# Kernel tuning notes

Measured on AMD Instinct MI355X. Metric: run time of the kernel, lower is better.

The kernel has to match this reference:

```python
import jax, jax.numpy as jnp
import numpy as np

N_NODES = 50000
N_EDGES = 500000
D_IN = 128
HID = 128
OUT = 2
N_REL = 4
BN_EPS = 1e-5


def setup_inputs() -> dict:
    key = jax.random.key(0)
    ks = jax.random.split(key, 14)
    s_in = 1.0 / np.sqrt(D_IN)
    s_h = 1.0 / np.sqrt(HID)
    return {
        "x": jax.random.normal(ks[0], (N_NODES, D_IN), jnp.float32),
        "edge_index": jax.random.randint(ks[1], (N_REL, 2, N_EDGES), 0, N_NODES, jnp.int32),
        "W1": jax.random.normal(ks[2], (N_REL, D_IN, HID), jnp.float32) * s_in,
        "b1": jax.random.normal(ks[3], (N_REL, HID), jnp.float32) * s_in,
        "W2": jax.random.normal(ks[4], (N_REL, HID, HID), jnp.float32) * s_h,
        "b2": jax.random.normal(ks[5], (N_REL, HID), jnp.float32) * s_h,
        "bn_gamma": jnp.ones((HID,), jnp.float32),
        "bn_beta": jnp.zeros((HID,), jnp.float32),
        "lin1_W": jax.random.normal(ks[6], (HID, HID), jnp.float32) * s_h,
        "lin1_b": jax.random.normal(ks[7], (HID,), jnp.float32) * s_h,
        "lin2_W": jax.random.normal(ks[8], (HID, OUT), jnp.float32) * s_h,
        "lin2_b": jax.random.normal(ks[9], (OUT,), jnp.float32) * s_h,
    }


def _gcn(x, ei, W, b):
    # GCNConv: D^-1/2 (A + I) D^-1/2 (X W) + b
    n = x.shape[0]
    h = x @ W                                    # [N, H]
    loops = jnp.arange(n, dtype=ei.dtype)
    src = jnp.concatenate([ei[0], loops])        # add self loops
    dst = jnp.concatenate([ei[1], loops])
    deg = jax.ops.segment_sum(jnp.ones(dst.shape, h.dtype), dst, num_segments=n)
    dinv = jnp.where(deg > 0, jax.lax.rsqrt(deg), 0.0)
    norm = dinv[src] * dinv[dst]                 # [E+N]
    msg = h[src] * norm[:, None]                 # gather + scale
    return jax.ops.segment_sum(msg, dst, num_segments=n) + b


def _hetero(x, edge_index, W, b):
    # HeteroConv with aggr='sum' over the 4 relation types (same src/dst node type)
    out = _gcn(x, edge_index[0], W[0], b[0])
    for r in range(1, N_REL):
        out = out + _gcn(x, edge_index[r], W[r], b[r])
    return out


def reference(x, edge_index, W1, b1, W2, b2, bn_gamma, bn_beta, lin1_W, lin1_b, lin2_W, lin2_b):
    h = jax.nn.relu(_hetero(x, edge_index, W1, b1))
    h = jax.nn.relu(_hetero(h, edge_index, W2, b2))
    # BatchNorm1d (batch statistics, biased variance)
    mean = h.mean(axis=0)
    var = h.var(axis=0)
    h = (h - mean) * jax.lax.rsqrt(var + BN_EPS) * bn_gamma + bn_beta
    h = jax.nn.relu(h @ lin1_W + lin1_b)
    # dropout is identity in eval
    return h @ lin2_W + lin2_b
```

## Files before the change

### kernel.cpp

```cpp
#include <hip/hip_runtime.h>
#include <math.h>

#define NN 50000
#define NE 500000
#define NREL 4
#define D 128
#define RSZ 512
#define NRANGE 98
#define NBK (NREL * NRANGE)
#define BCAP 6144
#define NCH 128
#define CH 3907
#define FCAP 96
#define CAST_BLKS 6250
#define TN 32
#define NPW 8
#define NTILE ((NN + TN - 1) / TN)
static constexpr float BN_EPS = 1e-5f;

typedef __attribute__((ext_vector_type(8))) _Float16 half8;
typedef __attribute__((ext_vector_type(4))) float f32x4;

__device__ __forceinline__ unsigned short f2h_bits(float f) {
    _Float16 h = (_Float16)f;
    return __builtin_bit_cast(unsigned short, h);
}
__device__ __forceinline__ float hi2f(unsigned p) {
    return (float)__builtin_bit_cast(_Float16, (unsigned short)(p >> 16));
}

__global__ __launch_bounds__(256) void k_pre(const float* __restrict__ x,
                                             const float* __restrict__ W1, const float* __restrict__ W2,
                                             const float* __restrict__ l1W, const float* __restrict__ b1,
                                             const float* __restrict__ b2,
                                             unsigned short* __restrict__ xb,
                                             unsigned short* __restrict__ Wt1,
                                             unsigned short* __restrict__ Wt2,
                                             unsigned short* __restrict__ Wt3,
                                             float* __restrict__ bs1, float* __restrict__ bs2,
                                             float* __restrict__ bnsum) {
    int blk = blockIdx.x, tid = threadIdx.x;
    if (blk < CAST_BLKS) {
        int i = blk * 256 + tid;
        float4 v = *(const float4*)(x + (size_t)i * 4);
        unsigned short u[4] = {f2h_bits(v.x), f2h_bits(v.y), f2h_bits(v.z), f2h_bits(v.w)};
        *(ushort4*)(xb + (size_t)i * 4) = *(ushort4*)u;
    } else if (blk < CAST_BLKS + 256) {
        int i = (blk - CAST_BLKS) * 256 + tid;
        int kk = i & 511, n = i >> 9;
        Wt1[n * 512 + kk] = f2h_bits(W1[kk * 128 + n]);
        Wt2[n * 512 + kk] = f2h_bits(W2[kk * 128 + n]);
    } else if (blk < CAST_BLKS + 320) {
        int i = (blk - CAST_BLKS - 256) * 256 + tid;
        int kk = i & 127, n = i >> 7;
        Wt3[n * 128 + kk] = f2h_bits(l1W[kk * 128 + n]);
    } else {
        if (tid < 128) {
            bs1[tid] = b1[tid] + b1[128 + tid] + b1[256 + tid] + b1[384 + tid];
            bs2[tid] = b2[tid] + b2[128 + tid] + b2[256 + tid] + b2[384 + tid];
        }
        bnsum[tid] = 0.f;
    }
}

__global__ __launch_bounds__(256) void k_bin(const int* __restrict__ ei,
                                             int* __restrict__ frag,
                                             int* __restrict__ cntg) {
    int c = blockIdx.x, r = blockIdx.y;
    const int* srcp = ei + r * 2 * NE;
    const int* dstp = srcp + NE;
    __shared__ int bins[NRANGE * FCAP];
    __shared__ int cnt[NRANGE];
    int tid = threadIdx.x;
    for (int i = tid; i < NRANGE; i += 256) cnt[i] = 0;
    __syncthreads();
    int e0 = c * CH, e1 = min(e0 + CH, NE);
    for (int e = e0 + tid; e < e1; e += 256) {
        int d = dstp[e];
        int s = srcp[e];
        int q = d >> 9;
        int pos = atomicAdd(&cnt[q], 1);
        if (pos < FCAP) bins[q * FCAP + pos] = s | ((d & 511) << 16);
    }
    __syncthreads();
    int w = tid >> 6, lane = tid & 63;
    for (int q = w; q < NRANGE; q += 4) {
        int k = min(cnt[q], FCAP);
        int gbase = ((r * NRANGE + q) * NCH + c) * FCAP;
        for (int i = lane; i < k; i += 64) frag[gbase + i] = bins[q * FCAP + i];
    }
    for (int q = tid; q < NRANGE; q += 256) cntg[(r * NRANGE + q) * NCH + c] = min(cnt[q], FCAP);
}

__global__ __launch_bounds__(512) void k_sortb(const int* __restrict__ frag,
                                               const int* __restrict__ cntg,
                                               unsigned short* __restrict__ csr,
                                               int* __restrict__ rstart,
                                               int* __restrict__ rend,
                                               float* __restrict__ dinv) {
    int q = blockIdx.x, r = blockIdx.y;
    int blk = r * NRANGE + q;
    int n0 = q * RSZ;
    int nrows = min(RSZ, NN - n0);
    __shared__ int cnts[NCH], cbase[NCH];
    __shared__ int stage[BCAP];
    __shared__ unsigned short csr_s[BCAP];
    __shared__ int hist[RSZ], off[RSZ], cnt2[RSZ];
    int tid = threadIdx.x;
    hist[tid] = 0;
    cnt2[tid] = 0;
    if (tid < NCH) cnts[tid] = cntg[blk * NCH + tid];
    __syncthreads();
    if (tid < NCH) cbase[tid] = cnts[tid];
    __syncthreads();
    for (int d = 1; d < NCH; d <<= 1) {
        int t = 0;
        if (tid < NCH && tid >= d) t = cbase[tid - d];
        __syncthreads();
        if (tid < NCH) cbase[tid] += t;
        __syncthreads();
    }
    if (tid < NCH) cbase[tid] -= cnts[tid];
    __syncthreads();
    int tot = cbase[NCH - 1] + cnts[NCH - 1];
    {
        int g = tid >> 2, l = tid & 3;
        int k = cnts[g], cb = cbase[g];
        int gbase = (blk * NCH + g) * FCAP;
        for (int i = l; i < k; i += 4)
            if (cb + i < BCAP) stage[cb + i] = frag[gbase + i];
    }
    __syncthreads();
    if (tot > BCAP) tot = BCAP;
    for (int i = tid; i < tot; i += 512) atomicAdd(&hist[(stage[i] >> 16) & 511], 1);
    __syncthreads();
    int h = hist[tid];
    if (tid < nrows) dinv[r * NN + n0 + tid] = rsqrtf((float)(h + 1));
    off[tid] = h;
    __syncthreads();
    for (int d = 1; d < RSZ; d <<= 1) {
        int t = (tid >= d) ? off[tid - d] : 0;
        __syncthreads();
        off[tid] += t;
        __syncthreads();
    }
    int excl = off[tid] - h;
    __syncthreads();
    off[tid] = excl;
    int base = blk * BCAP;
    if (tid < nrows) {
        rstart[r * NN + n0 + tid] = base + excl;
        rend[r * NN + n0 + tid] = base + excl + h;
    }
    __syncthreads();
    for (int i = tid; i < tot; i += 512) {
        int v = stage[i];
        int dl = (v >> 16) & 511;
        int p = atomicAdd(&cnt2[dl], 1);
        csr_s[off[dl] + p] = (unsigned short)(v & 0xFFFF);
    }
    __syncthreads();
    for (int i = tid; i < tot; i += 512) csr[base + i] = csr_s[i];
}

__global__ __launch_bounds__(256) void k_wei(const unsigned short* __restrict__ csr,
                                             const float* __restrict__ dinv,
                                             unsigned* __restrict__ wpack) {
    int gi = blockIdx.x * 256 + threadIdx.x;
    int r = gi / (NRANGE * BCAP);
    int s = csr[gi];
    float w = dinv[r * NN + min(s, NN - 1)];
    wpack[gi] = (unsigned)s | ((unsigned)f2h_bits(w) << 16);
}

template <bool STATS>
__global__ __launch_bounds__(256) void k_fused(const unsigned short* __restrict__ in,
                                               const unsigned* __restrict__ wpack,
                                               const int* __restrict__ rstart,
                                               const int* __restrict__ rend,
                                               const float* __restrict__ dinv,
                                               const unsigned short* __restrict__ Bt,
                                               const float* __restrict__ bias,
                                               unsigned short* __restrict__ C,
                                               float* __restrict__ bnsum) {
    __shared__ unsigned short A_s[TN * 512];
    int tid = threadIdx.x;
    int wave = tid >> 6, lane = tid & 63;
    int t = lane & 15;
    int base = lane & 48;
    int q = base >> 4;
    int tile = blockIdx.x;
    const half8* in8 = (const half8*)in;
    int nbq = q * NN;

    int row0 = wave * NPW;
    {
        int n0 = tile * TN + row0;
        int nc0 = min(n0, NN - 1);
        int sP = rstart[nbq + nc0];
        int eP = rend[nbq + nc0];
        float wP = dinv[nbq + nc0];
        half8 uP = in8[(size_t)nc0 * 16 + t];
        for (int i = 0; i < NPW; ++i) {
            int row = row0 + i;
            int n = tile * TN + row;
            bool valid = (n < NN);
            int start = sP;
            int deg = valid ? (eP - sP) : 0;
            float wn = valid ? wP : 0.f;
            half8 us = uP;
            if (i + 1 < NPW) {
                int nn = min(n + 1, NN - 1);
                sP = rstart[nbq + nn];
                eP = rend[nbq + nn];
                wP = dinv[nbq + nn];
                uP = in8[(size_t)nn * 16 + t];
            }
            int dm = deg;
            dm = max(dm, __shfl_xor(dm, 16));
            dm = max(dm, __shfl_xor(dm, 32));
            float a[8];
#pragma unroll
            for (int j = 0; j < 8; j++) a[j] = wn * (float)us[j];

            for (int w0 = 0; w0 < dm; w0 += 16) {
                int li = w0 + t;
                int gi = min(start + li, NBK * BCAP - 1);
                unsigned pv = wpack[gi];
                if (li >= deg) pv = 0u;
                unsigned p0 = __shfl(pv, base + 0), p1 = __shfl(pv, base + 1);
                unsigned p2 = __shfl(pv, base + 2), p3 = __shfl(pv, base + 3);
                unsigned p4 = __shfl(pv, base + 4), p5 = __shfl(pv, base + 5);
                unsigned p6 = __shfl(pv, base + 6), p7 = __shfl(pv, base + 7);
                {
                    half8 r0 = in8[(p0 & 0xFFFFu) * 16 + t];
                    half8 r1 = in8[(p1 & 0xFFFFu) * 16 + t];
                    half8 r2 = in8[(p2 & 0xFFFFu) * 16 + t];
                    half8 r3 = in8[(p3 & 0xFFFFu) * 16 + t];
                    half8 r4 = in8[(p4 & 0xFFFFu) * 16 + t];
                    half8 r5 = in8[(p5 & 0xFFFFu) * 16 + t];
                    half8 r6 = in8[(p6 & 0xFFFFu) * 16 + t];
                    half8 r7 = in8[(p7 & 0xFFFFu) * 16 + t];
                    float w0f = hi2f(p0), w1f = hi2f(p1), w2f = hi2f(p2), w3f = hi2f(p3);
                    float w4f = hi2f(p4), w5f = hi2f(p5), w6f = hi2f(p6), w7f = hi2f(p7);
#pragma unroll
                    for (int j = 0; j < 8; j++) a[j] = fmaf((float)r0[j], w0f, a[j]);
#pragma unroll
                    for (int j = 0; j < 8; j++) a[j] = fmaf((float)r1[j], w1f, a[j]);
#pragma unroll
                    for (int j = 0; j < 8; j++) a[j] = fmaf((float)r2[j], w2f, a[j]);
#pragma unroll
                    for (int j = 0; j < 8; j++) a[j] = fmaf((float)r3[j], w3f, a[j]);
#pragma unroll
                    for (int j = 0; j < 8; j++) a[j] = fmaf((float)r4[j], w4f, a[j]);
#pragma unroll
                    for (int j = 0; j < 8; j++) a[j] = fmaf((float)r5[j], w5f, a[j]);
#pragma unroll
                    for (int j = 0; j < 8; j++) a[j] = fmaf((float)r6[j], w6f, a[j]);
#pragma unroll
                    for (int j = 0; j < 8; j++) a[j] = fmaf((float)r7[j], w7f, a[j]);
                }
                if (w0 + 8 >= dm) continue;
                p0 = __shfl(pv, base + 8);  p1 = __shfl(pv, base + 9);
                p2 = __shfl(pv, base + 10); p3 = __shfl(pv, base + 11);
                p4 = __shfl(pv, base + 12); p5 = __shfl(pv, base + 13);
                p6 = __shfl(pv, base + 14); p7 = __shfl(pv, base + 15);
                {
                    half8 r0 = in8[(p0 & 0xFFFFu) * 16 + t];
                    half8 r1 = in8[(p1 & 0xFFFFu) * 16 + t];
                    half8 r2 = in8[(p2 & 0xFFFFu) * 16 + t];
                    half8 r3 = in8[(p3 & 0xFFFFu) * 16 + t];
                    half8 r4 = in8[(p4 & 0xFFFFu) * 16 + t];
                    half8 r5 = in8[(p5 & 0xFFFFu) * 16 + t];
                    half8 r6 = in8[(p6 & 0xFFFFu) * 16 + t];
                    half8 r7 = in8[(p7 & 0xFFFFu) * 16 + t];
                    float w0f = hi2f(p0), w1f = hi2f(p1), w2f = hi2f(p2), w3f = hi2f(p3);
                    float w4f = hi2f(p4), w5f = hi2f(p5), w6f = hi2f(p6), w7f = hi2f(p7);
#pragma unroll
                    for (int j = 0; j < 8; j++) a[j] = fmaf((float)r0[j], w0f, a[j]);
#pragma unroll
                    for (int j = 0; j < 8; j++) a[j] = fmaf((float)r1[j], w1f, a[j]);
#pragma unroll
                    for (int j = 0; j < 8; j++) a[j] = fmaf((float)r2[j], w2f, a[j]);
#pragma unroll
                    for (int j = 0; j < 8; j++) a[j] = fmaf((float)r3[j], w3f, a[j]);
#pragma unroll
                    for (int j = 0; j < 8; j++) a[j] = fmaf((float)r4[j], w4f, a[j]);
#pragma unroll
                    for (int j = 0; j < 8; j++) a[j] = fmaf((float)r5[j], w5f, a[j]);
#pragma unroll
                    for (int j = 0; j < 8; j++) a[j] = fmaf((float)r6[j], w6f, a[j]);
#pragma unroll
                    for (int j = 0; j < 8; j++) a[j] = fmaf((float)r7[j], w7f, a[j]);
                }
            }
            _Float16 ob[8];
#pragma unroll
            for (int j = 0; j < 8; j++) ob[j] = (_Float16)(wn * a[j]);
            int offb = row * 1024 + ((lane * 16) ^ ((row & 7) << 4));
            *(half8*)((char*)A_s + offb) = *(half8*)ob;
        }
    }
    __syncthreads();

    int ln = lane & 15, quad = lane >> 4;
    f32x4 acc[2][2];
#pragma unroll
    for (int a = 0; a < 2; a++)
#pragma unroll
        for (int b = 0; b < 2; b++) acc[a][b] = (f32x4){0.f, 0.f, 0.f, 0.f};
    size_t brow[2];
#pragma unroll
    for (int nf = 0; nf < 2; nf++) brow[nf] = (size_t)(wave * 32 + nf * 16 + ln) * 512;

    for (int k0 = 0; k0 < 512; k0 += 32) {
        int kofb = k0 * 2 + quad * 16;
        half8 af[2], bf[2];
#pragma unroll
        for (int mf = 0; mf < 2; mf++) {
            int rr = mf * 16 + ln;
            int offb = rr * 1024 + (kofb ^ ((rr & 7) << 4));
            af[mf] = *(const half8*)((const char*)A_s + offb);
        }
#pragma unroll
        for (int nf = 0; nf < 2; nf++) bf[nf] = *(const half8*)(Bt + brow[nf] + (kofb >> 1));
#pragma unroll
        for (int mf = 0; mf < 2; mf++)
#pragma unroll
            for (int nf = 0; nf < 2; nf++)
                acc[mf][nf] = __builtin_amdgcn_mfma_f32_16x16x32_f16(af[mf], bf[nf], acc[mf][nf], 0, 0, 0);
    }

    float bs[2];
#pragma unroll
    for (int nf = 0; nf < 2; nf++) bs[nf] = bias[wave * 32 + nf * 16 + ln];
    float sn[2] = {0.f, 0.f}, qn[2] = {0.f, 0.f};
#pragma unroll
    for (int mf = 0; mf < 2; mf++)
#pragma unroll
        for (int nf = 0; nf < 2; nf++)
#pragma unroll
            for (int rg = 0; rg < 4; rg++) {
                int m = tile * TN + mf * 16 + quad * 4 + rg;
                if (m < NN) {
                    float v = fmaxf(acc[mf][nf][rg] + bs[nf], 0.f);
                    if (STATS) { sn[nf] += v; qn[nf] += v * v; }
                    C[(size_t)m * 128 + wave * 32 + nf * 16 + ln] = f2h_bits(v);
                }
            }
    if (STATS) {
#pragma unroll
        for (int nf = 0; nf < 2; nf++) {
            float s = sn[nf], qq = qn[nf];
            s += __shfl_xor(s, 16); s += __shfl_xor(s, 32);
            qq += __shfl_xor(qq, 16); qq += __shfl_xor(qq, 32);
            if (quad == 0) {
                int col = wave * 32 + nf * 16 + ln;
                unsafeAtomicAdd(&bnsum[col], s);
                unsafeAtomicAdd(&bnsum[128 + col], qq);
            }
        }
    }
}

__global__ __launch_bounds__(256) void k_final(const unsigned short* __restrict__ R2,
                                               const float* __restrict__ bnsum,
                                               const float* __restrict__ gamma,
                                               const float* __restrict__ beta,
                                               const unsigned short* __restrict__ Wt3,
                                               const float* __restrict__ l1b,
                                               const float* __restrict__ l2W,
                                               const float* __restrict__ l2b,
                                               float* __restrict__ out) {
    __shared__ float bnp_s[256];
    int tid = threadIdx.x;
    if (tid < 128) {
        float mean = bnsum[tid] / (float)NN;
        float var = bnsum[128 + tid] / (float)NN - mean * mean;
        float sc = gamma[tid] * rsqrtf(var + BN_EPS);
        bnp_s[tid] = sc;
        bnp_s[128 + tid] = beta[tid] - mean * sc;
    }
    __syncthreads();
    int w = tid >> 6, lane = tid & 63;
    int ln = lane & 15, quad = lane >> 4;
    int mwave = blockIdx.x * 256 + w * 64;

    f32x4 acc[4][8];
#pragma unroll
    for (int a = 0; a < 4; a++)
#pragma unroll
        for (int b = 0; b < 8; b++) acc[a][b] = (f32x4){0.f, 0.f, 0.f, 0.f};

    size_t arow[4];
#pragma unroll
    for (int mf = 0; mf < 4; mf++) {
        int m = mwave + mf * 16 + ln;
        arow[mf] = (size_t)min(m, NN - 1) * 128;
    }
    size_t brow[8];
#pragma unroll
    for (int nf = 0; nf < 8; nf++) brow[nf] = (size_t)(nf * 16 + ln) * 128;

    for (int k0 = 0; k0 < 128; k0 += 32) {
        int kof = k0 + quad * 8;
        float scv[8], shv[8];
#pragma unroll
        for (int j = 0; j < 8; j++) {
            scv[j] = bnp_s[kof + j];
            shv[j] = bnp_s[128 + kof + j];
        }
        half8 af[4], bf[8];
#pragma unroll
        for (int mf = 0; mf < 4; mf++) {
            half8 rv = *(const half8*)(R2 + arow[mf] + kof);
            _Float16 ab[8];
#pragma unroll
            for (int j = 0; j < 8; j++)
                ab[j] = (_Float16)(fmaf((float)rv[j], scv[j], shv[j]));
            af[mf] = *(half8*)ab;
        }
#pragma unroll
        for (int nf = 0; nf < 8; nf++) bf[nf] = *(const half8*)(Wt3 + brow[nf] + kof);
#pragma unroll
        for (int mf = 0; mf < 4; mf++)
#pragma unroll
            for (int nf = 0; nf < 8; nf++)
                acc[mf][nf] = __builtin_amdgcn_mfma_f32_16x16x32_f16(af[mf], bf[nf], acc[mf][nf], 0, 0, 0);
    }

    float b1v[8], w0[8], w1[8];
#pragma unroll
    for (int nf = 0; nf < 8; nf++) {
        int n = nf * 16 + ln;
        b1v[nf] = l1b[n];
        w0[nf] = l2W[n * 2];
        w1[nf] = l2W[n * 2 + 1];
    }
    float ob0 = l2b[0], ob1 = l2b[1];
#pragma unroll
    for (int mf = 0; mf < 4; mf++)
#pragma unroll
        for (int rg = 0; rg < 4; rg++) {
            float p0 = 0.f, p1 = 0.f;
#pragma unroll
            for (int nf = 0; nf < 8; nf++) {
                float y = fmaxf(acc[mf][nf][rg] + b1v[nf], 0.f);
                p0 += y * w0[nf];
                p1 += y * w1[nf];
            }
            p0 += __shfl_xor(p0, 1); p0 += __shfl_xor(p0, 2);
            p0 += __shfl_xor(p0, 4); p0 += __shfl_xor(p0, 8);
            p1 += __shfl_xor(p1, 1); p1 += __shfl_xor(p1, 2);
            p1 += __shfl_xor(p1, 4); p1 += __shfl_xor(p1, 8);
            int m = mwave + mf * 16 + quad * 4 + rg;
            if (ln == 0 && m < NN) {
                out[(size_t)m * 2 + 0] = p0 + ob0;
                out[(size_t)m * 2 + 1] = p1 + ob1;
            }
        }
}

extern "C" void kernel_launch(void* const* d_in, const int* in_sizes, int n_in,
                              void* d_out, int out_size, void* d_ws, size_t ws_size,
                              hipStream_t stream) {
    const float* x = (const float*)d_in[0];
    const int* ei = (const int*)d_in[1];
    const float* W1 = (const float*)d_in[2];
    const float* b1 = (const float*)d_in[3];
    const float* W2 = (const float*)d_in[4];
    const float* b2 = (const float*)d_in[5];
    const float* gamma = (const float*)d_in[6];
    const float* beta = (const float*)d_in[7];
    const float* l1W = (const float*)d_in[8];
    const float* l1b = (const float*)d_in[9];
    const float* l2W = (const float*)d_in[10];
    const float* l2b = (const float*)d_in[11];
    float* out = (float*)d_out;

    char* ws = (char*)d_ws;
    size_t off = 0;
    auto alloc = [&](size_t bytes) {
        void* p = ws + off;
        off += (bytes + 255) & ~(size_t)255;
        return p;
    };
    float* dinv = (float*)alloc((size_t)NREL * NN * sizeof(float));
    int* rstart = (int*)alloc((size_t)NREL * NN * sizeof(int));
    int* rend = (int*)alloc((size_t)NREL * NN * sizeof(int));
    unsigned short* csr = (unsigned short*)alloc((size_t)NBK * BCAP * 2);
    unsigned* wpack = (unsigned*)alloc((size_t)NBK * BCAP * 4);
    unsigned short* xb = (unsigned short*)alloc((size_t)NN * D * 2);
    unsigned short* h1b = (unsigned short*)alloc((size_t)NN * D * 2);
    unsigned short* R2b = (unsigned short*)alloc((size_t)NN * D * 2);
    unsigned short* Wt1 = (unsigned short*)alloc(128 * 512 * 2);
    unsigned short* Wt2 = (unsigned short*)alloc(128 * 512 * 2);
    unsigned short* Wt3 = (unsigned short*)alloc(128 * 128 * 2);
    float* bs1 = (float*)alloc(128 * sizeof(float));
    float* bs2 = (float*)alloc(128 * sizeof(float));
    float* bnsum = (float*)alloc(256 * sizeof(float));
    int* frag = (int*)alloc((size_t)NREL * NRANGE * NCH * FCAP * 4);
    int* cntg = (int*)alloc((size_t)NREL * NRANGE * NCH * 4);

    k_pre<<<CAST_BLKS + 321, 256, 0, stream>>>(x, W1, W2, l1W, b1, b2, xb, Wt1, Wt2, Wt3,
                                               bs1, bs2, bnsum);
    dim3 bgrid(NCH, NREL);
    k_bin<<<bgrid, 256, 0, stream>>>(ei, frag, cntg);
    dim3 sgrid(NRANGE, NREL);
    k_sortb<<<sgrid, 512, 0, stream>>>(frag, cntg, csr, rstart, rend, dinv);
    k_wei<<<(NBK * BCAP) / 256, 256, 0, stream>>>(csr, dinv, wpack);

    k_fused<false><<<NTILE, 256, 0, stream>>>(xb, wpack, rstart, rend, dinv, Wt1, bs1, h1b, nullptr);
    k_fused<true><<<NTILE, 256, 0, stream>>>(h1b, wpack, rstart, rend, dinv, Wt2, bs2, R2b, bnsum);
    k_final<<<(NN + 255) / 256, 256, 0, stream>>>(R2b, bnsum, gamma, beta, Wt3, l1b, l2W, l2b, out);
}
```

Before: 358.9 us.

## Halve fused aggregate-GEMM node tile and prefetch first edge chunk of next node

Shrinks the fused gather+GEMM tile from 32 to 16 nodes per block (4 nodes per wave), doubling the block count. Removes bounds checks because 50000 divides evenly by 16. Prefetches the first wpack edge word for the next node along with its row metadata, to hide load latency in the gather loop. The smaller tile raises parallelism and load balance, but each block does half the MFMA work while still reloading the full B matrix, so weight traffic per node doubles.

```diff
diff --git a/kernel.cpp b/kernel.cpp
--- a/kernel.cpp
+++ b/kernel.cpp
@@ -13,9 +13,9 @@
 #define CH 3907
 #define FCAP 96
 #define CAST_BLKS 6250
-#define TN 32
-#define NPW 8
-#define NTILE ((NN + TN - 1) / TN)
+#define TN 16
+#define NPW 4
+#define NTILE (NN / TN)
 static constexpr float BN_EPS = 1e-5f;
 
 typedef __attribute__((ext_vector_type(8))) _Float16 half8;
@@ -27,6 +27,22 @@
 }
 __device__ __forceinline__ float hi2f(unsigned p) {
     return (float)__builtin_bit_cast(_Float16, (unsigned short)(p >> 16));
+}
+
+__device__ __forceinline__ void acc8(const half8* __restrict__ in8, int t, int src_lane,
+                                     unsigned pv, float a[8]) {
+    unsigned p[8];
+#pragma unroll
+    for (int e = 0; e < 8; e++) p[e] = __shfl(pv, src_lane + e);
+    half8 r[8];
+#pragma unroll
+    for (int e = 0; e < 8; e++) r[e] = in8[(p[e] & 0xFFFFu) * 16 + t];
+#pragma unroll
+    for (int e = 0; e < 8; e++) {
+        float w = hi2f(p[e]);
+#pragma unroll
+        for (int j = 0; j < 8; j++) a[j] = fmaf((float)r[e][j], w, a[j]);
+    }
 }
 
 __global__ __launch_bounds__(256) void k_pre(const float* __restrict__ x,
@@ -192,143 +208,73 @@
     int tile = blockIdx.x;
     const half8* in8 = (const half8*)in;
     int nbq = q * NN;
-
     int row0 = wave * NPW;
-    {
-        int n0 = tile * TN + row0;
-        int nc0 = min(n0, NN - 1);
-        int sP = rstart[nbq + nc0];
-        int eP = rend[nbq + nc0];
-        float wP = dinv[nbq + nc0];
-        half8 uP = in8[(size_t)nc0 * 16 + t];
-        for (int i = 0; i < NPW; ++i) {
-            int row = row0 + i;
-            int n = tile * TN + row;
-            bool valid = (n < NN);
-            int start = sP;
-            int deg = valid ? (eP - sP) : 0;
-            float wn = valid ? wP : 0.f;
-            half8 us = uP;
-            if (i + 1 < NPW) {
-                int nn = min(n + 1, NN - 1);
-                sP = rstart[nbq + nn];
-                eP = rend[nbq + nn];
-                wP = dinv[nbq + nn];
-                uP = in8[(size_t)nn * 16 + t];
+    int n0 = tile * TN + row0;
+
+    int sP = rstart[nbq + n0];
+    int eP = rend[nbq + n0];
+    float wP = dinv[nbq + n0];
+    half8 uP = in8[(size_t)n0 * 16 + t];
+    unsigned pvP = wpack[min(sP + t, NBK * BCAP - 1)];
+
+    for (int i = 0; i < NPW; ++i) {
+        int row = row0 + i;
+        int n = n0 + i;
+        int start = sP, deg = eP - sP;
+        float wn = wP;
+        half8 us = uP;
+        unsigned pv0 = (t < deg) ? pvP : 0u;
+        if (i + 1 < NPW) {
+            int nn = n + 1;
+            sP = rstart[nbq + nn];
+            eP = rend[nbq + nn];
+            wP = dinv[nbq + nn];
+            uP = in8[(size_t)nn * 16 + t];
+            pvP = wpack[min(sP + t, NBK * BCAP - 1)];
+        }
+        int dm = deg;
+        dm = max(dm, __shfl_xor(dm, 16));
+        dm = max(dm, __shfl_xor(dm, 32));
+        float a[8];
+#pragma unroll
+        for (int j = 0; j < 8; j++) a[j] = wn * (float)us[j];
+
+        for (int w0 = 0; w0 < dm; w0 += 16) {
+            unsigned pv;
+            if (w0 == 0) {
+                pv = pv0;
+            } else {
+                int li = w0 + t;
+                pv = wpack[min(start + li, NBK * BCAP - 1)];
+                if (li >= deg) pv = 0u;
             }
-            int dm = deg;
-            dm = max(dm, __shfl_xor(dm, 16));
-            dm = max(dm, __shfl_xor(dm, 32));
-            float a[8];
-#pragma unroll
-            for (int j = 0; j < 8; j++) a[j] = wn * (float)us[j];
-
-            for (int w0 = 0; w0 < dm; w0 += 16) {
-                int li = w0 + t;
-                int gi = min(start + li, NBK * BCAP - 1);
-                unsigned pv = wpack[gi];
-                if (li >= deg) pv = 0u;
-                unsigned p0 = __shfl(pv, base + 0), p1 = __shfl(pv, base + 1);
-                unsigned p2 = __shfl(pv, base + 2), p3 = __shfl(pv, base + 3);
-                unsigned p4 = __shfl(pv, base + 4), p5 = __shfl(pv, base + 5);
-                unsigned p6 = __shfl(pv, base + 6), p7 = __shfl(pv, base + 7);
-                {
-                    half8 r0 = in8[(p0 & 0xFFFFu) * 16 + t];
-                    half8 r1 = in8[(p1 & 0xFFFFu) * 16 + t];
-                    half8 r2 = in8[(p2 & 0xFFFFu) * 16 + t];
-                    half8 r3 = in8[(p3 & 0xFFFFu) * 16 + t];
-                    half8 r4 = in8[(p4 & 0xFFFFu) * 16 + t];
-                    half8 r5 = in8[(p5 & 0xFFFFu) * 16 + t];
-                    half8 r6 = in8[(p6 & 0xFFFFu) * 16 + t];
-                    half8 r7 = in8[(p7 & 0xFFFFu) * 16 + t];
-                    float w0f = hi2f(p0), w1f = hi2f(p1), w2f = hi2f(p2), w3f = hi2f(p3);
-                    float w4f = hi2f(p4), w5f = hi2f(p5), w6f = hi2f(p6), w7f = hi2f(p7);
-#pragma unroll
-                    for (int j = 0; j < 8; j++) a[j] = fmaf((float)r0[j], w0f, a[j]);
-#pragma unroll
-                    for (int j = 0; j < 8; j++) a[j] = fmaf((float)r1[j], w1f, a[j]);
-#pragma unroll
-                    for (int j = 0; j < 8; j++) a[j] = fmaf((float)r2[j], w2f, a[j]);
-#pragma unroll
-                    for (int j = 0; j < 8; j++) a[j] = fmaf((float)r3[j], w3f, a[j]);
-#pragma unroll
-                    for (int j = 0; j < 8; j++) a[j] = fmaf((float)r4[j], w4f, a[j]);
-#pragma unroll
-                    for (int j = 0; j < 8; j++) a[j] = fmaf((float)r5[j], w5f, a[j]);
-#pragma unroll
-                    for (int j = 0; j < 8; j++) a[j] = fmaf((float)r6[j], w6f, a[j]);
-#pragma unroll
-                    for (int j = 0; j < 8; j++) a[j] = fmaf((float)r7[j], w7f, a[j]);
-                }
-                if (w0 + 8 >= dm) continue;
-                p0 = __shfl(pv, base + 8);  p1 = __shfl(pv, base + 9);
-                p2 = __shfl(pv, base + 10); p3 = __shfl(pv, base + 11);
-                p4 = __shfl(pv, base + 12); p5 = __shfl(pv, base + 13);
-                p6 = __shfl(pv, base + 14); p7 = __shfl(pv, base + 15);
-                {
-                    half8 r0 = in8[(p0 & 0xFFFFu) * 16 + t];
-                    half8 r1 = in8[(p1 & 0xFFFFu) * 16 + t];
-                    half8 r2 = in8[(p2 & 0xFFFFu) * 16 + t];
-                    half8 r3 = in8[(p3 & 0xFFFFu) * 16 + t];
-                    half8 r4 = in8[(p4 & 0xFFFFu) * 16 + t];
-                    half8 r5 = in8[(p5 & 0xFFFFu) * 16 + t];
-                    half8 r6 = in8[(p6 & 0xFFFFu) * 16 + t];
-                    half8 r7 = in8[(p7 & 0xFFFFu) * 16 + t];
-                    float w0f = hi2f(p0), w1f = hi2f(p1), w2f = hi2f(p2), w3f = hi2f(p3);
-                    float w4f = hi2f(p4), w5f = hi2f(p5), w6f = hi2f(p6), w7f = hi2f(p7);
-#pragma unroll
-                    for (int j = 0; j < 8; j++) a[j] = fmaf((float)r0[j], w0f, a[j]);
-#pragma unroll
-                    for (int j = 0; j < 8; j++) a[j] = fmaf((float)r1[j], w1f, a[j]);
-#pragma unroll
-                    for (int j = 0; j < 8; j++) a[j] = fmaf((float)r2[j], w2f, a[j]);
-#pragma unroll
-                    for (int j = 0; j < 8; j++) a[j] = fmaf((float)r3[j], w3f, a[j]);
-#pragma unroll
-                    for (int j = 0; j < 8; j++) a[j] = fmaf((float)r4[j], w4f, a[j]);
-#pragma unroll
-                    for (int j = 0; j < 8; j++) a[j] = fmaf((float)r5[j], w5f, a[j]);
-#pragma unroll
-                    for (int j = 0; j < 8; j++) a[j] = fmaf((float)r6[j], w6f, a[j]);
-#pragma unroll
-                    for (int j = 0; j < 8; j++) a[j] = fmaf((float)r7[j], w7f, a[j]);
-                }
-            }
-            _Float16 ob[8];
-#pragma unroll
-            for (int j = 0; j < 8; j++) ob[j] = (_Float16)(wn * a[j]);
-            int offb = row * 1024 + ((lane * 16) ^ ((row & 7) << 4));
-            *(half8*)((char*)A_s + offb) = *(half8*)ob;
-        }
+            acc8(in8, t, base, pv, a);
+            if (w0 + 8 < dm) acc8(in8, t, base + 8, pv, a);
+        }
+        _Float16 ob[8];
+#pragma unroll
+        for (int j = 0; j < 8; j++) ob[j] = (_Float16)(wn * a[j]);
+        int offb = row * 1024 + ((lane * 16) ^ ((row & 7) << 4));
+        *(half8*)((char*)A_s + offb) = *(half8*)ob;
     }
     __syncthreads();
 
     int ln = lane & 15, quad = lane >> 4;
-    f32x4 acc[2][2];
-#pragma unroll
-    for (int a = 0; a < 2; a++)
-#pragma unroll
-        for (int b = 0; b < 2; b++) acc[a][b] = (f32x4){0.f, 0.f, 0.f, 0.f};
+    f32x4 acc[2];
+    acc[0] = (f32x4){0.f, 0.f, 0.f, 0.f};
+    acc[1] = (f32x4){0.f, 0.f, 0.f, 0.f};
     size_t brow[2];
 #pragma unroll
     for (int nf = 0; nf < 2; nf++) brow[nf] = (size_t)(wave * 32 + nf * 16 + ln) * 512;
 
     for (int k0 = 0; k0 < 512; k0 += 32) {
         int kofb = k0 * 2 + quad * 16;
-        half8 af[2], bf[2];
-#pragma unroll
-        for (int mf = 0; mf < 2; mf++) {
-            int rr = mf * 16 + ln;
-            int offb = rr * 1024 + (kofb ^ ((rr & 7) << 4));
-            af[mf] = *(const half8*)((const char*)A_s + offb);
-        }
-#pragma unroll
-        for (int nf = 0; nf < 2; nf++) bf[nf] = *(const half8*)(Bt + brow[nf] + (kofb >> 1));
-#pragma unroll
-        for (int mf = 0; mf < 2; mf++)
-#pragma unroll
-            for (int nf = 0; nf < 2; nf++)
-                acc[mf][nf] = __builtin_amdgcn_mfma_f32_16x16x32_f16(af[mf], bf[nf], acc[mf][nf], 0, 0, 0);
+        int offb = ln * 1024 + (kofb ^ ((ln & 7) << 4));
+        half8 af = *(const half8*)((const char*)A_s + offb);
+        half8 bf0 = *(const half8*)(Bt + brow[0] + (kofb >> 1));
+        half8 bf1 = *(const half8*)(Bt + brow[1] + (kofb >> 1));
+        acc[0] = __builtin_amdgcn_mfma_f32_16x16x32_f16(af, bf0, acc[0], 0, 0, 0);
+        acc[1] = __builtin_amdgcn_mfma_f32_16x16x32_f16(af, bf1, acc[1], 0, 0, 0);
     }
 
     float bs[2];
@@ -336,18 +282,14 @@
     for (int nf = 0; nf < 2; nf++) bs[nf] = bias[wave * 32 + nf * 16 + ln];
     float sn[2] = {0.f, 0.f}, qn[2] = {0.f, 0.f};
 #pragma unroll
-    for (int mf = 0; mf < 2; mf++)
-#pragma unroll
-        for (int nf = 0; nf < 2; nf++)
-#pragma unroll
-            for (int rg = 0; rg < 4; rg++) {
-                int m = tile * TN + mf * 16 + quad * 4 + rg;
-                if (m < NN) {
-                    float v = fmaxf(acc[mf][nf][rg] + bs[nf], 0.f);
-                    if (STATS) { sn[nf] += v; qn[nf] += v * v; }
-                    C[(size_t)m * 128 + wave * 32 + nf * 16 + ln] = f2h_bits(v);
-                }
-            }
+    for (int nf = 0; nf < 2; nf++)
+#pragma unroll
+        for (int rg = 0; rg < 4; rg++) {
+            int m = tile * TN + quad * 4 + rg;
+            float v = fmaxf(acc[nf][rg] + bs[nf], 0.f);
+            if (STATS) { sn[nf] += v; qn[nf] += v * v; }
+            C[(size_t)m * 128 + wave * 32 + nf * 16 + ln] = f2h_bits(v);
+        }
     if (STATS) {
 #pragma unroll
         for (int nf = 0; nf < 2; nf++) {
```

Result: no change. 362.9 us (+1.1%).
